# Kernel optimization log

Hardware: AMD Instinct MI355X
Metric: run time of the kernel (lower is better)

## Reference

```python
import jax, jax.numpy as jnp
import numpy as np
from jax import lax

B_, L, D, EXPAND, N, R, K = 2, 1024, 1024, 2, 16, 64, 4
ED = EXPAND * D


def setup_inputs() -> dict:
    key = jax.random.key(0)
    ks = jax.random.split(key, 8)
    x = jax.random.normal(ks[0], (B_, L, D), dtype=jnp.float32)
    in_proj_w = jax.random.normal(ks[1], (2 * ED, D), dtype=jnp.float32) * (D ** -0.5)
    in_proj_b = jnp.zeros((2 * ED,), jnp.float32)
    conv_w = jax.random.normal(ks[2], (ED, 1, K), dtype=jnp.float32) * (K ** -0.5)
    conv_b = jnp.zeros((ED,), jnp.float32)
    x_proj_w = jax.random.normal(ks[3], (R + 2 * N, ED), dtype=jnp.float32) * (ED ** -0.5)
    dt_proj_w = jax.random.uniform(ks[4], (ED, R), jnp.float32, -(R ** -0.5), R ** -0.5)
    # inverse-softplus of dt ~ U[log(dt_min), log(dt_max)] (matches torch init)
    dt = jnp.exp(jax.random.uniform(ks[5], (ED,), jnp.float32) * (np.log(0.1) - np.log(0.001)) + np.log(0.001))
    dt_proj_b = dt + jnp.log(-jnp.expm1(-dt))  # softplus^{-1}(dt)
    A_log = jnp.log(jnp.broadcast_to(jnp.arange(1, N + 1, dtype=jnp.float32), (ED, N)))
    D_param = jnp.ones((ED,), jnp.float32)
    out_proj_w = jax.random.normal(ks[6], (D, ED), dtype=jnp.float32) * (ED ** -0.5)
    return {"x": x, "in_proj_w": in_proj_w, "in_proj_b": in_proj_b, "conv_w": conv_w,
            "conv_b": conv_b, "x_proj_w": x_proj_w, "dt_proj_w": dt_proj_w,
            "dt_proj_b": dt_proj_b, "A_log": A_log, "D_param": D_param,
            "out_proj_w": out_proj_w}


def _mamba_fwd(x, in_proj_w, in_proj_b, conv_w, conv_b, x_proj_w, dt_proj_w,
               dt_proj_b, A_log, D_param, out_proj_w):
    xz = x @ in_proj_w.T + in_proj_b                       # (B, L, 2*ED)
    xc, z = jnp.split(xz, 2, axis=-1)                      # (B, L, ED) each
    # causal depthwise conv over time (pad left K-1, valid)
    xc = xc.transpose(0, 2, 1)                             # (B, ED, L)
    xc = lax.conv_general_dilated(xc, conv_w, window_strides=(1,),
                                  padding=[(K - 1, 0)], feature_group_count=ED)
    xc = xc + conv_b[None, :, None]
    xc = jax.nn.silu(xc.transpose(0, 2, 1))                # (B, L, ED)
    # SSM params
    A = -jnp.exp(A_log)                                    # (ED, N)
    dbc = xc @ x_proj_w.T                                  # (B, L, R+2N)
    dt, Bmat, Cmat = jnp.split(dbc, [R, R + N], axis=-1)
    dt = jax.nn.softplus(dt @ dt_proj_w.T + dt_proj_b)     # (B, L, ED)
    dA = jnp.exp(dt[..., None] * A)                        # (B, L, ED, N)
    dBx = (dt * xc)[..., None] * Bmat[:, :, None, :]       # (B, L, ED, N)
    # parallel scan: h_t = dA_t * h_{t-1} + dBx_t
    def combine(e1, e2):
        a1, b1 = e1
        a2, b2 = e2
        return a1 * a2, a2 * b1 + b2
    _, hs = lax.associative_scan(combine, (dA, dBx), axis=1)  # (B, L, ED, N)
    y = jnp.einsum('bln,blen->ble', Cmat, hs) + D_param * xc  # (B, L, ED)
    out = (y * jax.nn.silu(z)) @ out_proj_w.T                 # (B, L, D)
    return out


def reference(x, in_proj_w, in_proj_b, conv_w, conv_b, x_proj_w, dt_proj_w,
              dt_proj_b, A_log, D_param, out_proj_w):
    return _mamba_fwd(x, in_proj_w, in_proj_b, conv_w, conv_b, x_proj_w,
                      dt_proj_w, dt_proj_b, A_log, D_param, out_proj_w)
```

## Files before the change

kernel.cpp:

```cpp
#include <hip/hip_runtime.h>
#include <cstddef>


#define BL   2048
#define DIM  1024
#define ED   2048
#define NST  16
#define RLOW 64
#define CH   64
#define LC   16
#define SK   16
#define DBCN 196608

typedef __attribute__((ext_vector_type(4))) float   f32x4;
typedef __attribute__((ext_vector_type(8))) __bf16  bf16x8;
typedef __attribute__((ext_vector_type(8))) unsigned short us8;

__device__ __forceinline__ float silu_(float x) {
  return x / (1.f + __expf(-x));
}

__device__ __forceinline__ float softplus_(float x) {
  const float v = __logf(1.f + __expf(x));
  return (x > 20.f) ? x : v;
}

__device__ __forceinline__ unsigned short f2b(float x) {
  union { float f; unsigned int u; } v; v.f = x;
  unsigned int r = v.u + 0x7FFFu + ((v.u >> 16) & 1u);
  return (unsigned short)(r >> 16);
}

__device__ __forceinline__ float b2f(unsigned short u) {
  union { unsigned int i; float f; } v; v.i = (unsigned int)u << 16; return v.f;
}

__device__ __forceinline__ f32x4 mfma_bf16(us8 a, us8 b, f32x4 c) {
  return __builtin_amdgcn_mfma_f32_16x16x32_bf16(
      __builtin_bit_cast(bf16x8, a), __builtin_bit_cast(bf16x8, b), c, 0, 0, 0);
}

template <int N> __device__ __forceinline__ void vwaitN() {
  if constexpr (N == 0)      asm volatile("s_waitcnt vmcnt(0)" ::: "memory");
  else if constexpr (N == 3) asm volatile("s_waitcnt vmcnt(3)" ::: "memory");
  else if constexpr (N == 4) asm volatile("s_waitcnt vmcnt(4)" ::: "memory");
  else if constexpr (N == 6) asm volatile("s_waitcnt vmcnt(6)" ::: "memory");
  else if constexpr (N == 8) asm volatile("s_waitcnt vmcnt(8)" ::: "memory");
}

#define GLOAD_LDS16(gaddr, laddr)                                              \
  __builtin_amdgcn_global_load_lds(                                            \
      (const __attribute__((address_space(1))) unsigned int*)(gaddr),          \
      (__attribute__((address_space(3))) unsigned int*)(laddr), 16, 0, 0)

template <int BM, int BN, int ACT, bool OBF>
__global__ __launch_bounds__(256) void gemm_bf16(
    const unsigned short* __restrict__ A,
    const unsigned short* __restrict__ W,
    const float* __restrict__ bias,
    void* __restrict__ Cp, int ldc, int Nout, int Kloop, int lda, int sstride)
{
  constexpr int BK     = 32;
  constexpr int FM     = BM / 32;
  constexpr int FN     = BN / 32;
  constexpr int NLA    = BM / 64;
  constexpr int NLW    = BN / 64;
  constexpr int VPS    = NLA + NLW;
  constexpr int ABYTES = BM * BK * 2;
  constexpr int WBYTES = BN * BK * 2;
  __shared__ char smem[4 * (ABYTES + WBYTES)];

  const int tid  = threadIdx.x;
  const int w    = tid >> 6;
  const int lane = tid & 63;
  const int wr   = w >> 1, wc = w & 1;
  const int bm   = blockIdx.x * BM;
  const int bn   = blockIdx.y * BN;
  const int kb   = blockIdx.z * Kloop;

  f32x4 acc[FM][FN];
#pragma unroll
  for (int m = 0; m < FM; ++m)
#pragma unroll
    for (int n = 0; n < FN; ++n) acc[m][n] = (f32x4){0.f, 0.f, 0.f, 0.f};

  const int srow = (w << 4) | (lane & 15);
  const int kch  = lane >> 4;
  const int wofs = w * 1024;

  const unsigned short* Ag = A + (size_t)(bm + srow) * lda + kb + kch * 8;
  const unsigned short* Wg = W + (size_t)(bn + srow) * lda + kb + kch * 8;

#define STAGE(cur, k0)                                                         \
  {                                                                            \
    char* ab = smem + (cur) * (ABYTES + WBYTES);                               \
    char* wb = ab + ABYTES;                                                    \
    _Pragma("unroll")                                                          \
    for (int j = 0; j < NLA; ++j)                                              \
      GLOAD_LDS16(Ag + (size_t)(j * 64) * lda + (k0), ab + j * 4096 + wofs);   \
    _Pragma("unroll")                                                          \
    for (int j = 0; j < NLW; ++j)                                              \
      GLOAD_LDS16(Wg + (size_t)(j * 64) * lda + (k0), wb + j * 4096 + wofs);   \
  }

  const int NT = Kloop / BK;
  STAGE(0, 0);
  if (NT > 1) STAGE(1, BK);
  if (NT > 2) STAGE(2, 2 * BK);

  for (int t = 0; t < NT; ++t) {
    if (t <= NT - 3)      vwaitN<2 * VPS>();
    else if (t == NT - 2) vwaitN<VPS>();
    else                  vwaitN<0>();
    __builtin_amdgcn_sched_barrier(0);
    __builtin_amdgcn_s_barrier();
    __builtin_amdgcn_sched_barrier(0);
    if (t + 3 < NT) STAGE((t + 3) & 3, (size_t)(t + 3) * BK);

    const char* ab = smem + (t & 3) * (ABYTES + WBYTES);
    const char* wb = ab + ABYTES;
    us8 af[FM], wf[FN];
#pragma unroll
    for (int m = 0; m < FM; ++m)
      af[m] = *(const us8*)(ab + (wr * FM + m) * 1024 + lane * 16);
#pragma unroll
    for (int n = 0; n < FN; ++n)
      wf[n] = *(const us8*)(wb + (wc * FN + n) * 1024 + lane * 16);
#pragma unroll
    for (int m = 0; m < FM; ++m)
#pragma unroll
      for (int n = 0; n < FN; ++n)
        acc[m][n] = mfma_bf16(af[m], wf[n], acc[m][n]);
  }
#undef STAGE

  const int rbase = (lane >> 4) * 4;
  float* Cf = (float*)Cp + (size_t)blockIdx.z * sstride;
#pragma unroll
  for (int m = 0; m < FM; ++m) {
#pragma unroll
    for (int n = 0; n < FN; ++n) {
      const int col = bn + wc * (BN / 2) + n * 16 + (lane & 15);
      if (col < Nout) {
        const float bv = bias ? bias[col] : 0.f;
#pragma unroll
        for (int r = 0; r < 4; ++r) {
          const int row = bm + wr * (BM / 2) + m * 16 + rbase + r;
          float v = acc[m][n][r] + bv;
          if (ACT == 1) v = softplus_(v);
          if (OBF) ((unsigned short*)Cp)[(size_t)row * ldc + col] = f2b(v);
          else     Cf[(size_t)row * ldc + col] = v;
        }
      }
    }
  }
}

__global__ __launch_bounds__(256) void reduce_dbc_k(
    const float* __restrict__ par, float* __restrict__ dbc,
    unsigned short* __restrict__ dtA)
{
  const int i = blockIdx.x * 256 + threadIdx.x;
  float4 s = ((const float4*)par)[i];
#pragma unroll
  for (int sk = 1; sk < SK; ++sk) {
    float4 v = ((const float4*)(par + (size_t)sk * DBCN))[i];
    s.x += v.x; s.y += v.y; s.z += v.z; s.w += v.w;
  }
  ((float4*)dbc)[i] = s;
  const int row = i / 24, c4 = i % 24;
  if (c4 < 16) {
    ushort4 o;
    o.x = f2b(s.x); o.y = f2b(s.y); o.z = f2b(s.z); o.w = f2b(s.w);
    ((ushort4*)(dtA + (size_t)row * 64))[c4] = o;
  }
}

__global__ __launch_bounds__(256) void reduce_out_k(
    const float* __restrict__ par, float* __restrict__ out)
{
  const int i = blockIdx.x * 256 + threadIdx.x;
  float4 a = ((const float4*)par)[i];
#pragma unroll
  for (int k = 1; k < 4; ++k) {
    float4 b = ((const float4*)(par + (size_t)k * 2097152))[i];
    a.x += b.x; a.y += b.y; a.z += b.z; a.w += b.w;
  }
  ((float4*)out)[i] = a;
}

__global__ __launch_bounds__(256) void cvt_all_k(
    const float* __restrict__ x, const float* __restrict__ inw,
    const float* __restrict__ ow, const float* __restrict__ xpw,
    const float* __restrict__ dtw,
    unsigned short* __restrict__ xb, unsigned short* __restrict__ iwb,
    unsigned short* __restrict__ owb, unsigned short* __restrict__ xpwb,
    unsigned short* __restrict__ dtwb)
{
  const int i = blockIdx.x * 256 + threadIdx.x;
  const float* src; unsigned short* dst; int j;
  if (i < 524288)       { src = x;   dst = xb;  j = i; }
  else if (i < 1572864) { src = inw; dst = iwb; j = i - 524288; }
  else if (i < 2097152) { src = ow;  dst = owb; j = i - 1572864; }
  else if (i < 2162688) {
    j = i - 2097152;
    const int idx = j * 4;
    ushort4 o = {0, 0, 0, 0};
    if ((idx >> 11) < 96) {
      float4 v = *(const float4*)(xpw + idx);
      o.x = f2b(v.x); o.y = f2b(v.y); o.z = f2b(v.z); o.w = f2b(v.w);
    }
    *(ushort4*)(xpwb + idx) = o;
    return;
  } else                { src = dtw; dst = dtwb; j = i - 2162688; }
  float4 v = ((const float4*)src)[j];
  ushort4 o;
  o.x = f2b(v.x); o.y = f2b(v.y); o.z = f2b(v.z); o.w = f2b(v.w);
  ((ushort4*)dst)[j] = o;
}

__global__ __launch_bounds__(256) void conv_silu_k(
    const unsigned short* __restrict__ xzb, const float* __restrict__ cw,
    const float* __restrict__ cb, unsigned short* __restrict__ xcb)
{
  const int idx = blockIdx.x * 256 + threadIdx.x;
  const int row = idx >> 9;
  const int e   = (idx & 511) * 4;
  const int l   = row & 1023;
  const unsigned short* base = xzb + (size_t)(row - l) * (2 * ED) + e;

  float4 cbv = *(const float4*)(cb + e);
  float a0 = cbv.x, a1 = cbv.y, a2 = cbv.z, a3 = cbv.w;
#pragma unroll
  for (int k = 0; k < 4; ++k) {
    const int ls = l - 3 + k;
    if (ls >= 0) {
      ushort4 u = *(const ushort4*)(base + (size_t)ls * (2 * ED));
      a0 += cw[(size_t)(e + 0) * 4 + k] * b2f(u.x);
      a1 += cw[(size_t)(e + 1) * 4 + k] * b2f(u.y);
      a2 += cw[(size_t)(e + 2) * 4 + k] * b2f(u.z);
      a3 += cw[(size_t)(e + 3) * 4 + k] * b2f(u.w);
    }
  }
  ushort4 o;
  o.x = f2b(silu_(a0)); o.y = f2b(silu_(a1));
  o.z = f2b(silu_(a2)); o.w = f2b(silu_(a3));
  *(ushort4*)(xcb + (size_t)row * ED + e) = o;
}

__global__ __launch_bounds__(256, 4) void scan_phase1(
    const unsigned short* __restrict__ dt, const unsigned short* __restrict__ xcb,
    const float* __restrict__ dbc, const float* __restrict__ A_log,
    float* __restrict__ aprod_o, float* __restrict__ bfin_o)
{
  const int g  = blockIdx.x * 256 + threadIdx.x;
  const int e  = g & (ED - 1);
  const int bc = g >> 11;
  const int b  = bc >> 6;
  const int c  = bc & (CH - 1);
  const size_t rowbase = (size_t)b * 1024 + (size_t)c * LC;

  __shared__ float4 sB[LC][4];
  if (threadIdx.x < LC * 4) {
    const int row = threadIdx.x >> 2, q = threadIdx.x & 3;
    sB[row][q] = ((const float4*)(dbc + (rowbase + row) * 96 + RLOW))[q];
  }
  __syncthreads();

  float Aen[NST];
  {
    const float4* Ap = (const float4*)(A_log + (size_t)e * NST);
#pragma unroll
    for (int q = 0; q < 4; ++q) {
      float4 v = Ap[q];
      Aen[q*4+0] = -__expf(v.x); Aen[q*4+1] = -__expf(v.y);
      Aen[q*4+2] = -__expf(v.z); Aen[q*4+3] = -__expf(v.w);
    }
  }

  float dtv[LC], dxv[LC];
#pragma unroll
  for (int i = 0; i < LC; ++i) dtv[i] = b2f(dt[(rowbase + i) * ED + e]);
#pragma unroll
  for (int i = 0; i < LC; ++i)
    dxv[i] = dtv[i] * b2f(xcb[(rowbase + i) * ED + e]);

  float h[NST], ap[NST];
#pragma unroll
  for (int n = 0; n < NST; ++n) { h[n] = 0.f; ap[n] = 1.f; }

  for (int i = 0; i < LC; ++i) {
    float Bv[NST];
#pragma unroll
    for (int q = 0; q < 4; ++q) {
      float4 v = sB[i][q];
      Bv[q*4+0]=v.x; Bv[q*4+1]=v.y; Bv[q*4+2]=v.z; Bv[q*4+3]=v.w;
    }
#pragma unroll
    for (int n = 0; n < NST; ++n) {
      const float dA = __expf(dtv[i] * Aen[n]);
      ap[n] *= dA;
      h[n] = fmaf(dA, h[n], dxv[i] * Bv[n]);
    }
  }

  const size_t obase = ((size_t)(b * ED + e) * CH + c) * NST;
  float4* ao = (float4*)(aprod_o + obase);
  float4* bo = (float4*)(bfin_o + obase);
#pragma unroll
  for (int q = 0; q < 4; ++q) {
    ao[q] = make_float4(ap[q*4+0], ap[q*4+1], ap[q*4+2], ap[q*4+3]);
    bo[q] = make_float4(h[q*4+0],  h[q*4+1],  h[q*4+2],  h[q*4+3]);
  }
}

__global__ __launch_bounds__(256) void scan_phase2(
    const float* __restrict__ aprod, float* __restrict__ bfin)
{
  const int be   = blockIdx.x * 4 + (threadIdx.x >> 6);
  const int lane = threadIdx.x & 63;
  const size_t base = (size_t)be * CH * NST;

  float Aa[NST], Bb[NST];
  {
    const float4* ap4 = (const float4*)(aprod + base);
    const float4* bp4 = (const float4*)(bfin + base);
#pragma unroll
    for (int q = 0; q < 4; ++q) {
      float4 v = ap4[lane * 4 + q];
      Aa[q*4+0]=v.x; Aa[q*4+1]=v.y; Aa[q*4+2]=v.z; Aa[q*4+3]=v.w;
      float4 w = bp4[lane * 4 + q];
      Bb[q*4+0]=w.x; Bb[q*4+1]=w.y; Bb[q*4+2]=w.z; Bb[q*4+3]=w.w;
    }
  }

#pragma unroll
  for (int d = 1; d < 64; d <<= 1) {
#pragma unroll
    for (int r = 0; r < NST; ++r) {
      const float aP = __shfl_up(Aa[r], d);
      const float bP = __shfl_up(Bb[r], d);
      if (lane >= d) {
        Bb[r] = fmaf(Aa[r], bP, Bb[r]);
        Aa[r] *= aP;
      }
    }
  }

#pragma unroll
  for (int r = 0; r < NST; ++r) {
    const float hs = __shfl_up(Bb[r], 1);
    Bb[r] = (lane == 0) ? 0.f : hs;
  }

  float4* ob4 = (float4*)(bfin + base);
#pragma unroll
  for (int q = 0; q < 4; ++q)
    ob4[lane * 4 + q] = make_float4(Bb[q*4+0], Bb[q*4+1], Bb[q*4+2], Bb[q*4+3]);
}

__global__ __launch_bounds__(256, 4) void scan_phase3(
    const unsigned short* __restrict__ dt, const unsigned short* __restrict__ xcb,
    const float* __restrict__ dbc, const float* __restrict__ A_log,
    const float* __restrict__ Dp, const unsigned short* __restrict__ xzb,
    const float* __restrict__ hst, unsigned short* __restrict__ ygb)
{
  const int g  = blockIdx.x * 256 + threadIdx.x;
  const int e  = g & (ED - 1);
  const int bc = g >> 11;
  const int b  = bc >> 6;
  const int c  = bc & (CH - 1);
  const size_t rowbase = (size_t)b * 1024 + (size_t)c * LC;

  __shared__ float4 sBC[LC][8];
  if (threadIdx.x < LC * 8) {
    const int row = threadIdx.x >> 3, q = threadIdx.x & 7;
    sBC[row][q] = ((const float4*)(dbc + (rowbase + row) * 96 + RLOW))[q];
  }
  __syncthreads();

  float Aen[NST];
  {
    const float4* Ap = (const float4*)(A_log + (size_t)e * NST);
#pragma unroll
    for (int q = 0; q < 4; ++q) {
      float4 v = Ap[q];
      Aen[q*4+0] = -__expf(v.x); Aen[q*4+1] = -__expf(v.y);
      Aen[q*4+2] = -__expf(v.z); Aen[q*4+3] = -__expf(v.w);
    }
  }

  float dtv[LC], xcv[LC];
#pragma unroll
  for (int i = 0; i < LC; ++i) dtv[i] = b2f(dt[(rowbase + i) * ED + e]);
#pragma unroll
  for (int i = 0; i < LC; ++i) xcv[i] = b2f(xcb[(rowbase + i) * ED + e]);

  float h[NST];
  {
    const float4* Hp = (const float4*)(hst + ((size_t)(b * ED + e) * CH + c) * NST);
#pragma unroll
    for (int q = 0; q < 4; ++q) {
      float4 v = Hp[q];
      h[q*4+0]=v.x; h[q*4+1]=v.y; h[q*4+2]=v.z; h[q*4+3]=v.w;
    }
  }

  const float De = Dp[e];
  for (int i = 0; i < LC; ++i) {
    const size_t rr = rowbase + i;
    float Bv[NST], Cv[NST];
#pragma unroll
    for (int q = 0; q < 4; ++q) {
      float4 v = sBC[i][q];
      Bv[q*4+0]=v.x; Bv[q*4+1]=v.y; Bv[q*4+2]=v.z; Bv[q*4+3]=v.w;
      float4 w = sBC[i][q + 4];
      Cv[q*4+0]=w.x; Cv[q*4+1]=w.y; Cv[q*4+2]=w.z; Cv[q*4+3]=w.w;
    }
    const float dx = dtv[i] * xcv[i];
    float y = 0.f;
#pragma unroll
    for (int n = 0; n < NST; ++n) {
      const float dA = __expf(dtv[i] * Aen[n]);
      h[n] = fmaf(dA, h[n], dx * Bv[n]);
      y = fmaf(Cv[n], h[n], y);
    }
    y = fmaf(De, xcv[i], y);
    const float zf = b2f(xzb[rr * (2 * ED) + ED + e]);
    ygb[rr * ED + e] = f2b(y * silu_(zf));
  }
}

extern "C" void kernel_launch(void* const* d_in, const int* in_sizes, int n_in,
                              void* d_out, int out_size, void* d_ws, size_t ws_size,
                              hipStream_t stream) {
  const float* x         = (const float*)d_in[0];
  const float* in_w      = (const float*)d_in[1];
  const float* in_b      = (const float*)d_in[2];
  const float* conv_w    = (const float*)d_in[3];
  const float* conv_b    = (const float*)d_in[4];
  const float* xproj_w   = (const float*)d_in[5];
  const float* dtproj_w  = (const float*)d_in[6];
  const float* dtproj_b  = (const float*)d_in[7];
  const float* A_log     = (const float*)d_in[8];
  const float* D_param   = (const float*)d_in[9];
  const float* outproj_w = (const float*)d_in[10];
  float* out = (float*)d_out;

  float* ws    = (float*)d_ws;
  float* dbc   = ws;
  unsigned short* dtbu = (unsigned short*)(dbc + 196608);
  float* aprod = (float*)(dtbu + 4194304);
  float* bfin  = aprod + 4194304;
  float* parx  = bfin  + 4194304;
  unsigned short* xzb  = (unsigned short*)(parx + 3145728);
  unsigned short* xb   = xzb  + 8388608;
  unsigned short* iwb  = xb   + 2097152;
  unsigned short* owb  = iwb  + 4194304;
  unsigned short* xpwb = owb  + 2097152;
  unsigned short* xcb  = xpwb + 262144;
  unsigned short* ygb  = xcb  + 4194304;
  unsigned short* dtA  = ygb  + 4194304;
  unsigned short* dtwb = dtA  + 131072;
  float* paro  = aprod;

  const dim3 blk(256);

  cvt_all_k<<<dim3(2195456 / 256), blk, 0, stream>>>(
      x, in_w, outproj_w, xproj_w, dtproj_w, xb, iwb, owb, xpwb, dtwb);

  gemm_bf16<128, 128, 0, true><<<dim3(BL / 128, 4096 / 128), blk, 0, stream>>>(
      xb, iwb, in_b, xzb, 2 * ED, 2 * ED, DIM, DIM, 0);

  conv_silu_k<<<dim3((BL * (ED / 4)) / 256), blk, 0, stream>>>(
      xzb, conv_w, conv_b, xcb);

  gemm_bf16<128, 128, 0, false><<<dim3(BL / 128, 1, SK), blk, 0, stream>>>(
      xcb, xpwb, nullptr, parx, 96, 96, ED / SK, ED, DBCN);
  reduce_dbc_k<<<dim3(DBCN / 4 / 256), blk, 0, stream>>>(parx, dbc, dtA);

  gemm_bf16<64, 128, 1, true><<<dim3(BL / 64, ED / 128), blk, 0, stream>>>(
      dtA, dtwb, dtproj_b, dtbu, ED, ED, RLOW, RLOW, 0);

  scan_phase1<<<dim3((2 * CH * ED) / 256), blk, 0, stream>>>(
      dtbu, xcb, dbc, A_log, aprod, bfin);
  scan_phase2<<<dim3((2 * ED) / 4), blk, 0, stream>>>(aprod, bfin);
  scan_phase3<<<dim3((2 * CH * ED) / 256), blk, 0, stream>>>(
      dtbu, xcb, dbc, A_log, D_param, xzb, bfin, ygb);

  gemm_bf16<128, 128, 0, false><<<dim3(BL / 128, 1024 / 128, 4), blk, 0, stream>>>(
      ygb, owb, nullptr, paro, DIM, DIM, ED / 4, ED, 2097152);
  reduce_out_k<<<dim3(2097152 / 4 / 256), blk, 0, stream>>>(paro, out);
}
```

Baseline: 192.1 us.

## Halve scan chunk count to 32 and add XCD-aware block swizzle for in_proj GEMM

The chunked selective scan now uses 32 chunks of 32 timesteps instead of 64 chunks of 16. This halves the aprod/bfin intermediate traffic and the phase-2 shuffle depth, at the cost of half as many threads in phases 1 and 3 and longer serial loops per thread, which are processed in two 16-step halves to limit register pressure. Phase 2 masks off the upper half of each wavefront. The in_proj GEMM also gets a block-index swizzle that groups tiles by mod-8 to improve L2 locality across the chiplet dies.

```diff
diff --git a/kernel.cpp b/kernel.cpp
--- a/kernel.cpp
+++ b/kernel.cpp
@@ -7,8 +7,8 @@
 #define ED   2048
 #define NST  16
 #define RLOW 64
-#define CH   64
-#define LC   16
+#define CH   32
+#define LC   32
 #define SK   16
 #define DBCN 196608
 
@@ -53,7 +53,7 @@
       (const __attribute__((address_space(1))) unsigned int*)(gaddr),          \
       (__attribute__((address_space(3))) unsigned int*)(laddr), 16, 0, 0)
 
-template <int BM, int BN, int ACT, bool OBF>
+template <int BM, int BN, int ACT, bool OBF, int SWZ>
 __global__ __launch_bounds__(256) void gemm_bf16(
     const unsigned short* __restrict__ A,
     const unsigned short* __restrict__ W,
@@ -74,8 +74,17 @@
   const int w    = tid >> 6;
   const int lane = tid & 63;
   const int wr   = w >> 1, wc = w & 1;
-  const int bm   = blockIdx.x * BM;
-  const int bn   = blockIdx.y * BN;
+
+  int bx = blockIdx.x, by = blockIdx.y;
+  if (SWZ) {
+    const int nwg  = gridDim.x * gridDim.y;
+    const int flat = by * gridDim.x + bx;
+    const int nid  = (flat & 7) * (nwg >> 3) + (flat >> 3);
+    bx = nid % gridDim.x;
+    by = nid / gridDim.x;
+  }
+  const int bm   = bx * BM;
+  const int bn   = by * BN;
   const int kb   = blockIdx.z * Kloop;
 
   f32x4 acc[FM][FN];
@@ -256,7 +265,7 @@
   const int g  = blockIdx.x * 256 + threadIdx.x;
   const int e  = g & (ED - 1);
   const int bc = g >> 11;
-  const int b  = bc >> 6;
+  const int b  = bc >> 5;
   const int c  = bc & (CH - 1);
   const size_t rowbase = (size_t)b * 1024 + (size_t)c * LC;
 
@@ -278,29 +287,32 @@
     }
   }
 
-  float dtv[LC], dxv[LC];
-#pragma unroll
-  for (int i = 0; i < LC; ++i) dtv[i] = b2f(dt[(rowbase + i) * ED + e]);
-#pragma unroll
-  for (int i = 0; i < LC; ++i)
-    dxv[i] = dtv[i] * b2f(xcb[(rowbase + i) * ED + e]);
-
   float h[NST], ap[NST];
 #pragma unroll
   for (int n = 0; n < NST; ++n) { h[n] = 0.f; ap[n] = 1.f; }
 
-  for (int i = 0; i < LC; ++i) {
-    float Bv[NST];
-#pragma unroll
-    for (int q = 0; q < 4; ++q) {
-      float4 v = sB[i][q];
-      Bv[q*4+0]=v.x; Bv[q*4+1]=v.y; Bv[q*4+2]=v.z; Bv[q*4+3]=v.w;
-    }
-#pragma unroll
-    for (int n = 0; n < NST; ++n) {
-      const float dA = __expf(dtv[i] * Aen[n]);
-      ap[n] *= dA;
-      h[n] = fmaf(dA, h[n], dxv[i] * Bv[n]);
+#pragma unroll
+  for (int half = 0; half < 2; ++half) {
+    float dtv[16], dxv[16];
+#pragma unroll
+    for (int i = 0; i < 16; ++i)
+      dtv[i] = b2f(dt[(rowbase + half * 16 + i) * ED + e]);
+#pragma unroll
+    for (int i = 0; i < 16; ++i)
+      dxv[i] = dtv[i] * b2f(xcb[(rowbase + half * 16 + i) * ED + e]);
+    for (int i = 0; i < 16; ++i) {
+      float Bv[NST];
+#pragma unroll
+      for (int q = 0; q < 4; ++q) {
+        float4 v = sB[half * 16 + i][q];
+        Bv[q*4+0]=v.x; Bv[q*4+1]=v.y; Bv[q*4+2]=v.z; Bv[q*4+3]=v.w;
+      }
+#pragma unroll
+      for (int n = 0; n < NST; ++n) {
+        const float dA = __expf(dtv[i] * Aen[n]);
+        ap[n] *= dA;
+        h[n] = fmaf(dA, h[n], dxv[i] * Bv[n]);
+      }
     }
   }
 
@@ -322,7 +334,7 @@
   const size_t base = (size_t)be * CH * NST;
 
   float Aa[NST], Bb[NST];
-  {
+  if (lane < CH) {
     const float4* ap4 = (const float4*)(aprod + base);
     const float4* bp4 = (const float4*)(bfin + base);
 #pragma unroll
@@ -332,15 +344,18 @@
       float4 w = bp4[lane * 4 + q];
       Bb[q*4+0]=w.x; Bb[q*4+1]=w.y; Bb[q*4+2]=w.z; Bb[q*4+3]=w.w;
     }
-  }
-
-#pragma unroll
-  for (int d = 1; d < 64; d <<= 1) {
+  } else {
+#pragma unroll
+    for (int r = 0; r < NST; ++r) { Aa[r] = 0.f; Bb[r] = 0.f; }
+  }
+
+#pragma unroll
+  for (int d = 1; d < CH; d <<= 1) {
 #pragma unroll
     for (int r = 0; r < NST; ++r) {
       const float aP = __shfl_up(Aa[r], d);
       const float bP = __shfl_up(Bb[r], d);
-      if (lane >= d) {
+      if (lane >= d && lane < CH) {
         Bb[r] = fmaf(Aa[r], bP, Bb[r]);
         Aa[r] *= aP;
       }
@@ -353,10 +368,12 @@
     Bb[r] = (lane == 0) ? 0.f : hs;
   }
 
-  float4* ob4 = (float4*)(bfin + base);
-#pragma unroll
-  for (int q = 0; q < 4; ++q)
-    ob4[lane * 4 + q] = make_float4(Bb[q*4+0], Bb[q*4+1], Bb[q*4+2], Bb[q*4+3]);
+  if (lane < CH) {
+    float4* ob4 = (float4*)(bfin + base);
+#pragma unroll
+    for (int q = 0; q < 4; ++q)
+      ob4[lane * 4 + q] = make_float4(Bb[q*4+0], Bb[q*4+1], Bb[q*4+2], Bb[q*4+3]);
+  }
 }
 
 __global__ __launch_bounds__(256, 4) void scan_phase3(
@@ -368,12 +385,12 @@
   const int g  = blockIdx.x * 256 + threadIdx.x;
   const int e  = g & (ED - 1);
   const int bc = g >> 11;
-  const int b  = bc >> 6;
+  const int b  = bc >> 5;
   const int c  = bc & (CH - 1);
   const size_t rowbase = (size_t)b * 1024 + (size_t)c * LC;
 
   __shared__ float4 sBC[LC][8];
-  if (threadIdx.x < LC * 8) {
+  {
     const int row = threadIdx.x >> 3, q = threadIdx.x & 7;
     sBC[row][q] = ((const float4*)(dbc + (rowbase + row) * 96 + RLOW))[q];
   }
@@ -390,12 +407,6 @@
     }
   }
 
-  float dtv[LC], xcv[LC];
-#pragma unroll
-  for (int i = 0; i < LC; ++i) dtv[i] = b2f(dt[(rowbase + i) * ED + e]);
-#pragma unroll
-  for (int i = 0; i < LC; ++i) xcv[i] = b2f(xcb[(rowbase + i) * ED + e]);
-
   float h[NST];
   {
     const float4* Hp = (const float4*)(hst + ((size_t)(b * ED + e) * CH + c) * NST);
@@ -407,27 +418,37 @@
   }
 
   const float De = Dp[e];
-  for (int i = 0; i < LC; ++i) {
-    const size_t rr = rowbase + i;
-    float Bv[NST], Cv[NST];
-#pragma unroll
-    for (int q = 0; q < 4; ++q) {
-      float4 v = sBC[i][q];
-      Bv[q*4+0]=v.x; Bv[q*4+1]=v.y; Bv[q*4+2]=v.z; Bv[q*4+3]=v.w;
-      float4 w = sBC[i][q + 4];
-      Cv[q*4+0]=w.x; Cv[q*4+1]=w.y; Cv[q*4+2]=w.z; Cv[q*4+3]=w.w;
-    }
-    const float dx = dtv[i] * xcv[i];
-    float y = 0.f;
-#pragma unroll
-    for (int n = 0; n < NST; ++n) {
-      const float dA = __expf(dtv[i] * Aen[n]);
-      h[n] = fmaf(dA, h[n], dx * Bv[n]);
-      y = fmaf(Cv[n], h[n], y);
-    }
-    y = fmaf(De, xcv[i], y);
-    const float zf = b2f(xzb[rr * (2 * ED) + ED + e]);
-    ygb[rr * ED + e] = f2b(y * silu_(zf));
+#pragma unroll
+  for (int half = 0; half < 2; ++half) {
+    float dtv[16], xcv[16];
+#pragma unroll
+    for (int i = 0; i < 16; ++i)
+      dtv[i] = b2f(dt[(rowbase + half * 16 + i) * ED + e]);
+#pragma unroll
+    for (int i = 0; i < 16; ++i)
+      xcv[i] = b2f(xcb[(rowbase + half * 16 + i) * ED + e]);
+    for (int i = 0; i < 16; ++i) {
+      const size_t rr = rowbase + half * 16 + i;
+      float Bv[NST], Cv[NST];
+#pragma unroll
+      for (int q = 0; q < 4; ++q) {
+        float4 v = sBC[half * 16 + i][q];
+        Bv[q*4+0]=v.x; Bv[q*4+1]=v.y; Bv[q*4+2]=v.z; Bv[q*4+3]=v.w;
+        float4 w = sBC[half * 16 + i][q + 4];
+        Cv[q*4+0]=w.x; Cv[q*4+1]=w.y; Cv[q*4+2]=w.z; Cv[q*4+3]=w.w;
+      }
+      const float dx = dtv[i] * xcv[i];
+      float y = 0.f;
+#pragma unroll
+      for (int n = 0; n < NST; ++n) {
+        const float dA = __expf(dtv[i] * Aen[n]);
+        h[n] = fmaf(dA, h[n], dx * Bv[n]);
+        y = fmaf(Cv[n], h[n], y);
+      }
+      y = fmaf(De, xcv[i], y);
+      const float zf = b2f(xzb[rr * (2 * ED) + ED + e]);
+      ygb[rr * ED + e] = f2b(y * silu_(zf));
+    }
   }
 }
 
@@ -451,8 +472,8 @@
   float* dbc   = ws;
   unsigned short* dtbu = (unsigned short*)(dbc + 196608);
   float* aprod = (float*)(dtbu + 4194304);
-  float* bfin  = aprod + 4194304;
-  float* parx  = bfin  + 4194304;
+  float* bfin  = aprod + 2097152;
+  float* parx  = bfin  + 2097152;
   unsigned short* xzb  = (unsigned short*)(parx + 3145728);
   unsigned short* xb   = xzb  + 8388608;
   unsigned short* iwb  = xb   + 2097152;
@@ -469,17 +490,17 @@
   cvt_all_k<<<dim3(2195456 / 256), blk, 0, stream>>>(
       x, in_w, outproj_w, xproj_w, dtproj_w, xb, iwb, owb, xpwb, dtwb);
 
-  gemm_bf16<128, 128, 0, true><<<dim3(BL / 128, 4096 / 128), blk, 0, stream>>>(
+  gemm_bf16<128, 128, 0, true, 1><<<dim3(BL / 128, 4096 / 128), blk, 0, stream>>>(
       xb, iwb, in_b, xzb, 2 * ED, 2 * ED, DIM, DIM, 0);
 
   conv_silu_k<<<dim3((BL * (ED / 4)) / 256), blk, 0, stream>>>(
       xzb, conv_w, conv_b, xcb);
 
-  gemm_bf16<128, 128, 0, false><<<dim3(BL / 128, 1, SK), blk, 0, stream>>>(
+  gemm_bf16<128, 128, 0, false, 0><<<dim3(BL / 128, 1, SK), blk, 0, stream>>>(
       xcb, xpwb, nullptr, parx, 96, 96, ED / SK, ED, DBCN);
   reduce_dbc_k<<<dim3(DBCN / 4 / 256), blk, 0, stream>>>(parx, dbc, dtA);
 
-  gemm_bf16<64, 128, 1, true><<<dim3(BL / 64, ED / 128), blk, 0, stream>>>(
+  gemm_bf16<64, 128, 1, true, 0><<<dim3(BL / 64, ED / 128), blk, 0, stream>>>(
       dtA, dtwb, dtproj_b, dtbu, ED, ED, RLOW, RLOW, 0);
 
   scan_phase1<<<dim3((2 * CH * ED) / 256), blk, 0, stream>>>(
@@ -488,7 +509,7 @@
   scan_phase3<<<dim3((2 * CH * ED) / 256), blk, 0, stream>>>(
       dtbu, xcb, dbc, A_log, D_param, xzb, bfin, ygb);
 
-  gemm_bf16<128, 128, 0, false><<<dim3(BL / 128, 1024 / 128, 4), blk, 0, stream>>>(
+  gemm_bf16<128, 128, 0, false, 0><<<dim3(BL / 128, 1024 / 128, 4), blk, 0, stream>>>(
       ygb, owb, nullptr, paro, DIM, DIM, ED / 4, ED, 2097152);
   reduce_out_k<<<dim3(2097152 / 4 / 256), blk, 0, stream>>>(paro, out);
 }
```

Result: slower. 296.0 us (+54.1%).
